# Optimization experiments

Hardware: AMD Instinct MI355X
Metric: run time of the kernel (lower is better)

Reference implementation:

```python
import jax, jax.numpy as jnp
import numpy as np

B, N, F_IN, H, E = 8, 10000, 128, 128, 160000


def setup_inputs() -> dict:
    key = jax.random.key(0)
    ks = jax.random.split(key, 6)
    x = jax.random.normal(ks[0], (B, N, F_IN), dtype=jnp.float32)
    edge_index = jax.random.randint(ks[1], (2, E), 0, N, dtype=jnp.int64)
    # GCNConv params (glorot-ish scale), LayerNorm affine params
    W1 = jax.random.normal(ks[2], (F_IN, H), dtype=jnp.float32) / np.sqrt(F_IN)
    b1 = jnp.zeros((H,), dtype=jnp.float32)
    W2 = jax.random.normal(ks[3], (H, H), dtype=jnp.float32) / np.sqrt(H)
    b2 = jnp.zeros((H,), dtype=jnp.float32)
    ln_w = jnp.ones((H,), dtype=jnp.float32)
    ln_b = jnp.zeros((H,), dtype=jnp.float32)
    return {"x": x, "edge_index": edge_index, "W1": W1, "b1": b1,
            "W2": W2, "b2": b2, "ln_w": ln_w, "ln_b": ln_b}


def reference(x, edge_index, W1, b1, W2, b2, ln_w, ln_b):
    # x: [B, N, F]; edge_index: [2, E] shared across batch (tiled per graph
    # in the original via node offsets -> equivalent to vmapping over batch).
    n = x.shape[1]
    loops = jnp.arange(n, dtype=edge_index.dtype)
    src = jnp.concatenate([edge_index[0], loops])  # add self-loops (GCNConv default)
    dst = jnp.concatenate([edge_index[1], loops])
    # symmetric degree normalization: deg over targets with self-loops
    deg = jax.ops.segment_sum(jnp.ones(dst.shape[0], dtype=x.dtype), dst, num_segments=n)
    dinv = jnp.where(deg > 0, jax.lax.rsqrt(deg), 0.0)
    w_e = dinv[src] * dinv[dst]  # [E+N] per-edge norm

    def gcn_agg(h):  # h: [B, N, H] -> gather, scale, scatter-add
        msg = h[:, src, :] * w_e[None, :, None]  # [B, E+N, H]
        return jax.vmap(lambda m: jax.ops.segment_sum(m, dst, num_segments=n))(msg)

    h1 = jax.nn.relu(gcn_agg(x @ W1) + b1)
    h2 = gcn_agg(h1 @ W2) + b2
    # LayerNorm over last dim (eps=1e-5, torch default)
    mu = jnp.mean(h2, axis=-1, keepdims=True)
    var = jnp.mean(jnp.square(h2 - mu), axis=-1, keepdims=True)
    out = (h2 - mu) * jax.lax.rsqrt(var + 1e-5) * ln_w + ln_b
    return out  # [B, N, H]
```

## Files before the change

kernel.cpp:

```cpp
#include <hip/hip_runtime.h>
#include <hip/hip_bf16.h>

#define NNODES 10000
#define NB 8
#define NF 128
#define NE 160000

typedef __attribute__((ext_vector_type(8))) short  short8;
typedef __attribute__((ext_vector_type(8))) unsigned short ushort8;
typedef __attribute__((ext_vector_type(4))) float  f32x4;

__device__ __forceinline__ unsigned short f2b(float f) {
    union { float f; unsigned u; } v; v.f = f;
    unsigned r = v.u + 0x7FFF + ((v.u >> 16) & 1);
    return (unsigned short)(r >> 16);
}
__device__ __forceinline__ unsigned int f2b2(float a, float b) {
    union { __hip_bfloat162 h; unsigned int u; } v;
    v.h = __float22bfloat162_rn(make_float2(a, b));
    return v.u;
}
__device__ __forceinline__ float b2f_lo(unsigned u) {
    union { unsigned u; float f; } v; v.u = u << 16; return v.f;
}
__device__ __forceinline__ float b2f_hi(unsigned u) {
    union { unsigned u; float f; } v; v.u = u & 0xffff0000u; return v.f;
}


__global__ void k_count(const int* __restrict__ ei, int* __restrict__ cnt) {
    int e = blockIdx.x * blockDim.x + threadIdx.x;
    if (e < NE) atomicAdd(&cnt[ei[NE + e]], 1);
}

__global__ __launch_bounds__(1024) void k_scan(const int* __restrict__ cnt,
                                               int* __restrict__ row_ptr,
                                               float* __restrict__ dinv) {
    __shared__ int wsum[16];
    const int t = threadIdx.x;
    const int lane = t & 63, wv = t >> 6;
    const int CH = 10;
    int lo = t * CH;
    int hi = min(lo + CH, NNODES);
    int c10[CH];
    int s = 0;
    for (int i = lo; i < hi; i++) {
        int c = cnt[i];
        c10[i - lo] = c;
        dinv[i] = rsqrtf((float)(c + 1));
        s += c;
    }
    int v = s;
    #pragma unroll
    for (int m = 1; m < 64; m <<= 1) {
        int o = __shfl_up(v, m);
        if (lane >= m) v += o;
    }
    if (lane == 63) wsum[wv] = v;
    __syncthreads();
    if (t < 16) {
        int w = wsum[t];
        #pragma unroll
        for (int m = 1; m < 16; m <<= 1) {
            int o = __shfl_up(w, m);
            if (t >= m) w += o;
        }
        wsum[t] = w;
    }
    __syncthreads();
    int base = v - s + (wv ? wsum[wv - 1] : 0);
    for (int i = lo; i < hi; i++) { row_ptr[i] = base; base += c10[i - lo]; }
    if (t == 1023) row_ptr[NNODES] = wsum[15];
}

__global__ void k_scatter(const int* __restrict__ ei, const int* __restrict__ row_ptr,
                          int* __restrict__ fill, const float* __restrict__ dinv,
                          unsigned int* __restrict__ edge) {
    int e = blockIdx.x * blockDim.x + threadIdx.x;
    if (e >= NE) return;
    int s = ei[e];
    int d = ei[NE + e];
    int pos = row_ptr[d] + atomicAdd(&fill[d], 1);
    edge[pos] = (unsigned)s | ((unsigned)f2b(dinv[s] * dinv[d]) << 16);
}

__global__ void k_wt2(const float* __restrict__ W1, unsigned short* __restrict__ Wt1,
                      const float* __restrict__ W2, unsigned short* __restrict__ Wt2) {
    int bid = blockIdx.x;
    const float* W = (bid < 64) ? W1 : W2;
    unsigned short* Wt = (bid < 64) ? Wt1 : Wt2;
    int id = (bid & 63) * 256 + threadIdx.x;
    int n = id >> 7, k = id & 127;
    Wt[(size_t)n * 128 + k] = f2b(W[(size_t)k * 128 + n]);
}

template <bool ABF16>
__global__ __launch_bounds__(256) void k_mm_mfma(const void* __restrict__ Ap,
                                                 const unsigned short* __restrict__ Wt,
                                                 unsigned short* __restrict__ Cn) {
    __shared__ unsigned short clds[128 * 136];
    const int t = threadIdx.x;
    const int wid = t >> 6, lane = t & 63;
    const int quad = lane >> 4, l16 = lane & 15;
    const int m0 = blockIdx.x * 128 + (wid & 1) * 64;
    const int nb = (wid >> 1) * 64;
    const int kq = quad * 8;

    f32x4 acc[4][4] = {};

    #pragma unroll
    for (int ks = 0; ks < 128; ks += 32) {
        short8 af[4];
        #pragma unroll
        for (int ni = 0; ni < 4; ni++)
            af[ni] = *(const short8*)(Wt + (size_t)(nb + ni * 16 + l16) * 128 + ks + kq);
        short8 bf[4];
        #pragma unroll
        for (int mi = 0; mi < 4; mi++) {
            const size_t row = (size_t)(m0 + mi * 16 + l16);
            if constexpr (ABF16) {
                bf[mi] = *(const short8*)((const unsigned short*)Ap + row * 128 + ks + kq);
            } else {
                const float* p = (const float*)Ap + row * 128 + ks + kq;
                float4 u0 = *(const float4*)p;
                float4 u1 = *(const float4*)(p + 4);
                union { uint4 u4; short8 s8; } cv;
                cv.u4.x = f2b2(u0.x, u0.y); cv.u4.y = f2b2(u0.z, u0.w);
                cv.u4.z = f2b2(u1.x, u1.y); cv.u4.w = f2b2(u1.z, u1.w);
                bf[mi] = cv.s8;
            }
        }
        #pragma unroll
        for (int mi = 0; mi < 4; mi++)
            #pragma unroll
            for (int ni = 0; ni < 4; ni++)
                acc[mi][ni] = __builtin_amdgcn_mfma_f32_16x16x32_bf16(
                    af[ni], bf[mi], acc[mi][ni], 0, 0, 0);
    }

    {
        const int rbase = (wid & 1) * 64;
        #pragma unroll
        for (int mi = 0; mi < 4; mi++) {
            int rr = rbase + mi * 16 + l16;
            #pragma unroll
            for (int ni = 0; ni < 4; ni++) {
                uint2 p;
                p.x = f2b2(acc[mi][ni][0], acc[mi][ni][1]);
                p.y = f2b2(acc[mi][ni][2], acc[mi][ni][3]);
                *(uint2*)(clds + rr * 136 + nb + ni * 16 + quad * 4) = p;
            }
        }
    }
    __syncthreads();
    {
        const int r = t >> 1, h = t & 1;
        size_t gm = (size_t)blockIdx.x * 128 + r;
        unsigned short* dst = Cn + gm * 128 + h * 64;
        const unsigned short* srow = clds + r * 136 + h * 64;
        #pragma unroll
        for (int i = 0; i < 8; i++)
            *(ushort8*)(dst + i * 8) = *(const ushort8*)(srow + i * 8);
    }
}


__global__ __launch_bounds__(256) void k_agg_relu(const unsigned int* __restrict__ hNu,
                                                  const float* __restrict__ bias,
                                                  const int* __restrict__ row_ptr,
                                                  const unsigned int* __restrict__ edge,
                                                  const float* __restrict__ dinv,
                                                  unsigned int* __restrict__ h1u) {
    const int t = threadIdx.x;
    const int b = blockIdx.x & 7;
    const int g = blockIdx.x >> 3;
    const int wid = __builtin_amdgcn_readfirstlane(t >> 6);
    const int lane = t & 63;
    const int n = g * 4 + wid;

    const unsigned int* base = hNu + (size_t)b * NNODES * 64 + lane;
    float di = dinv[n];
    float wself = di * di;
    unsigned int u = base[(size_t)n * 64];
    float a0 = b2f_lo(u) * wself;
    float a1 = b2f_hi(u) * wself;

    int e = row_ptr[n], e1 = row_ptr[n + 1];
    for (; e + 8 <= e1; e += 8) {
        unsigned int E[8];
        #pragma unroll
        for (int j = 0; j < 8; j++) E[j] = edge[e + j];
        unsigned int U[8];
        #pragma unroll
        for (int j = 0; j < 8; j++) U[j] = base[(size_t)(E[j] & 0xffffu) * 64];
        #pragma unroll
        for (int j = 0; j < 8; j++) {
            float w = b2f_hi(E[j]);
            a0 = fmaf(b2f_lo(U[j]), w, a0);
            a1 = fmaf(b2f_hi(U[j]), w, a1);
        }
    }
    for (; e + 4 <= e1; e += 4) {
        unsigned int E[4];
        #pragma unroll
        for (int j = 0; j < 4; j++) E[j] = edge[e + j];
        unsigned int U[4];
        #pragma unroll
        for (int j = 0; j < 4; j++) U[j] = base[(size_t)(E[j] & 0xffffu) * 64];
        #pragma unroll
        for (int j = 0; j < 4; j++) {
            float w = b2f_hi(E[j]);
            a0 = fmaf(b2f_lo(U[j]), w, a0);
            a1 = fmaf(b2f_hi(U[j]), w, a1);
        }
    }
    for (; e < e1; ++e) {
        unsigned int E = edge[e];
        float w = b2f_hi(E);
        unsigned int uu = base[(size_t)(E & 0xffffu) * 64];
        a0 = fmaf(b2f_lo(uu), w, a0);
        a1 = fmaf(b2f_hi(uu), w, a1);
    }
    a0 = fmaxf(a0 + bias[lane * 2], 0.f);
    a1 = fmaxf(a1 + bias[lane * 2 + 1], 0.f);
    __builtin_nontemporal_store(f2b2(a0, a1), &h1u[((size_t)b * NNODES + n) * 64 + lane]);
}

__global__ __launch_bounds__(256) void k_agg_ln(const unsigned int* __restrict__ hNu,
                                                const float* __restrict__ bias,
                                                const int* __restrict__ row_ptr,
                                                const unsigned int* __restrict__ edge,
                                                const float* __restrict__ dinv,
                                                const float* __restrict__ ln_w,
                                                const float* __restrict__ ln_b,
                                                float* __restrict__ out) {
    const int t = threadIdx.x;
    const int b = blockIdx.x & 7;
    const int g = blockIdx.x >> 3;
    const int wid = __builtin_amdgcn_readfirstlane(t >> 6);
    const int lane = t & 63;
    const int n = g * 4 + wid;

    const unsigned int* base = hNu + (size_t)b * NNODES * 64 + lane;
    float di = dinv[n];
    float wself = di * di;
    unsigned int u = base[(size_t)n * 64];
    float a0 = b2f_lo(u) * wself;
    float a1 = b2f_hi(u) * wself;

    int e = row_ptr[n], e1 = row_ptr[n + 1];
    for (; e + 8 <= e1; e += 8) {
        unsigned int E[8];
        #pragma unroll
        for (int j = 0; j < 8; j++) E[j] = edge[e + j];
        unsigned int U[8];
        #pragma unroll
        for (int j = 0; j < 8; j++) U[j] = base[(size_t)(E[j] & 0xffffu) * 64];
        #pragma unroll
        for (int j = 0; j < 8; j++) {
            float w = b2f_hi(E[j]);
            a0 = fmaf(b2f_lo(U[j]), w, a0);
            a1 = fmaf(b2f_hi(U[j]), w, a1);
        }
    }
    for (; e + 4 <= e1; e += 4) {
        unsigned int E[4];
        #pragma unroll
        for (int j = 0; j < 4; j++) E[j] = edge[e + j];
        unsigned int U[4];
        #pragma unroll
        for (int j = 0; j < 4; j++) U[j] = base[(size_t)(E[j] & 0xffffu) * 64];
        #pragma unroll
        for (int j = 0; j < 4; j++) {
            float w = b2f_hi(E[j]);
            a0 = fmaf(b2f_lo(U[j]), w, a0);
            a1 = fmaf(b2f_hi(U[j]), w, a1);
        }
    }
    for (; e < e1; ++e) {
        unsigned int E = edge[e];
        float w = b2f_hi(E);
        unsigned int uu = base[(size_t)(E & 0xffffu) * 64];
        a0 = fmaf(b2f_lo(uu), w, a0);
        a1 = fmaf(b2f_hi(uu), w, a1);
    }
    a0 += bias[lane * 2];
    a1 += bias[lane * 2 + 1];

    float s1 = a0 + a1;
    float s2 = a0 * a0 + a1 * a1;
    #pragma unroll
    for (int m = 1; m < 64; m <<= 1) {
        s1 += __shfl_xor(s1, m);
        s2 += __shfl_xor(s2, m);
    }
    float mu = s1 * (1.f / NF);
    float var = s2 * (1.f / NF) - mu * mu;
    float rs = rsqrtf(var + 1e-5f);

    float o0 = (a0 - mu) * rs * ln_w[lane * 2] + ln_b[lane * 2];
    float o1 = (a1 - mu) * rs * ln_w[lane * 2 + 1] + ln_b[lane * 2 + 1];
    float* dst = out + ((size_t)b * NNODES + n) * 128 + lane * 2;
    __builtin_nontemporal_store(o0, dst);
    __builtin_nontemporal_store(o1, dst + 1);
}


extern "C" void kernel_launch(void* const* d_in, const int* in_sizes, int n_in,
                              void* d_out, int out_size, void* d_ws, size_t ws_size,
                              hipStream_t stream) {
    const float* x    = (const float*)d_in[0];
    const int*   ei   = (const int*)d_in[1];
    const float* W1   = (const float*)d_in[2];
    const float* b1   = (const float*)d_in[3];
    const float* W2   = (const float*)d_in[4];
    const float* b2   = (const float*)d_in[5];
    const float* ln_w = (const float*)d_in[6];
    const float* ln_b = (const float*)d_in[7];
    float* out = (float*)d_out;

    char* ws = (char*)d_ws;
    int*            cnt     = (int*)(ws + 0);
    int*            fill    = (int*)(ws + 40192);
    int*            row_ptr = (int*)(ws + 80384);
    float*          dinv    = (float*)(ws + 120832);
    unsigned int*   edge    = (unsigned int*)(ws + 161024);
    unsigned short* hA16    = (unsigned short*)(ws + 1441024);
    unsigned short* h1b     = (unsigned short*)(ws + 21921024);
    unsigned short* Wt1     = (unsigned short*)cnt;
    unsigned short* Wt2     = (unsigned short*)fill;

    hipMemsetAsync(ws, 0, 80384, stream);
    k_count  <<<(NE + 255) / 256, 256, 0, stream>>>(ei, cnt);
    k_scan   <<<1, 1024, 0, stream>>>(cnt, row_ptr, dinv);
    k_scatter<<<(NE + 255) / 256, 256, 0, stream>>>(ei, row_ptr, fill, dinv, edge);
    k_wt2    <<<128, 256, 0, stream>>>(W1, Wt1, W2, Wt2);

    k_mm_mfma<false><<<(NB * NNODES) / 128, 256, 0, stream>>>(x, Wt1, hA16);
    k_agg_relu<<<(NNODES / 4) * NB, 256, 0, stream>>>((const unsigned int*)hA16, b1,
                                                      row_ptr, edge, dinv,
                                                      (unsigned int*)h1b);

    k_mm_mfma<true><<<(NB * NNODES) / 128, 256, 0, stream>>>(h1b, Wt2, hA16);
    k_agg_ln<<<(NNODES / 4) * NB, 256, 0, stream>>>((const unsigned int*)hA16, b2,
                                                    row_ptr, edge, dinv,
                                                    ln_w, ln_b, out);
}
```

Baseline: 233.4 us.

## Assign aggregation batches to XCDs via atomic work claiming for L2 locality

```diff
diff --git a/kernel.cpp b/kernel.cpp
--- a/kernel.cpp
+++ b/kernel.cpp
@@ -5,10 +5,13 @@
 #define NB 8
 #define NF 128
 #define NE 160000
+#define NGRP 625
 
 typedef __attribute__((ext_vector_type(8))) short  short8;
 typedef __attribute__((ext_vector_type(8))) unsigned short ushort8;
 typedef __attribute__((ext_vector_type(4))) float  f32x4;
+
+#define HWREG_XCC_ID (20 | (0 << 6) | ((4 - 1) << 11))
 
 __device__ __forceinline__ unsigned short f2b(float f) {
     union { float f; unsigned u; } v; v.f = f;
@@ -28,9 +31,21 @@
 }
 
 
-__global__ void k_count(const int* __restrict__ ei, int* __restrict__ cnt) {
-    int e = blockIdx.x * blockDim.x + threadIdx.x;
-    if (e < NE) atomicAdd(&cnt[ei[NE + e]], 1);
+__global__ void k_count_wt(const int* __restrict__ ei, int* __restrict__ cnt,
+                           const float* __restrict__ W1, unsigned short* __restrict__ Wt1,
+                           const float* __restrict__ W2, unsigned short* __restrict__ Wt2) {
+    int bid = blockIdx.x;
+    if (bid < 625) {
+        int e = bid * 256 + threadIdx.x;
+        atomicAdd(&cnt[ei[NE + e]], 1);
+    } else {
+        int id2 = (bid - 625) * 256 + threadIdx.x;
+        const float* W = (id2 < 16384) ? W1 : W2;
+        unsigned short* Wt = (id2 < 16384) ? Wt1 : Wt2;
+        int id = id2 & 16383;
+        int n = id >> 7, k = id & 127;
+        Wt[n * 128 + k] = f2b(W[k * 128 + n]);
+    }
 }
 
 __global__ __launch_bounds__(1024) void k_scan(const int* __restrict__ cnt,
@@ -84,16 +99,6 @@
     edge[pos] = (unsigned)s | ((unsigned)f2b(dinv[s] * dinv[d]) << 16);
 }
 
-__global__ void k_wt2(const float* __restrict__ W1, unsigned short* __restrict__ Wt1,
-                      const float* __restrict__ W2, unsigned short* __restrict__ Wt2) {
-    int bid = blockIdx.x;
-    const float* W = (bid < 64) ? W1 : W2;
-    unsigned short* Wt = (bid < 64) ? Wt1 : Wt2;
-    int id = (bid & 63) * 256 + threadIdx.x;
-    int n = id >> 7, k = id & 127;
-    Wt[(size_t)n * 128 + k] = f2b(W[(size_t)k * 128 + n]);
-}
-
 template <bool ABF16>
 __global__ __launch_bounds__(256) void k_mm_mfma(const void* __restrict__ Ap,
                                                  const unsigned short* __restrict__ Wt,
@@ -165,65 +170,86 @@
 }
 
 
+__device__ __forceinline__ int claim_item(int* ctr) {
+    int xcc = __builtin_amdgcn_s_getreg(HWREG_XCC_ID) & 7;
+    int got = -1;
+    for (int k = 0; k < 8; k++) {
+        int b = (xcc + k) & 7;
+        int idx = atomicAdd(&ctr[b], 1);
+        if (idx < NGRP) { got = b * NGRP + idx; break; }
+    }
+    return got;
+}
+
 __global__ __launch_bounds__(256) void k_agg_relu(const unsigned int* __restrict__ hNu,
                                                   const float* __restrict__ bias,
                                                   const int* __restrict__ row_ptr,
                                                   const unsigned int* __restrict__ edge,
                                                   const float* __restrict__ dinv,
-                                                  unsigned int* __restrict__ h1u) {
-    const int t = threadIdx.x;
-    const int b = blockIdx.x & 7;
-    const int g = blockIdx.x >> 3;
-    const int wid = __builtin_amdgcn_readfirstlane(t >> 6);
-    const int lane = t & 63;
-    const int n = g * 4 + wid;
+                                                  unsigned int* __restrict__ h1u,
+                                                  int* __restrict__ ctr) {
+    __shared__ int s_item;
+    if (threadIdx.x == 0) s_item = claim_item(ctr);
+    __syncthreads();
+    const int item = s_item;
+    if (item < 0) return;
+    const int b = item / NGRP;
+    const int g = item - b * NGRP;
+    const int wid = __builtin_amdgcn_readfirstlane(threadIdx.x >> 6);
+    const int lane = threadIdx.x & 63;
 
     const unsigned int* base = hNu + (size_t)b * NNODES * 64 + lane;
-    float di = dinv[n];
-    float wself = di * di;
-    unsigned int u = base[(size_t)n * 64];
-    float a0 = b2f_lo(u) * wself;
-    float a1 = b2f_hi(u) * wself;
-
-    int e = row_ptr[n], e1 = row_ptr[n + 1];
-    for (; e + 8 <= e1; e += 8) {
-        unsigned int E[8];
-        #pragma unroll
-        for (int j = 0; j < 8; j++) E[j] = edge[e + j];
-        unsigned int U[8];
-        #pragma unroll
-        for (int j = 0; j < 8; j++) U[j] = base[(size_t)(E[j] & 0xffffu) * 64];
-        #pragma unroll
-        for (int j = 0; j < 8; j++) {
-            float w = b2f_hi(E[j]);
-            a0 = fmaf(b2f_lo(U[j]), w, a0);
-            a1 = fmaf(b2f_hi(U[j]), w, a1);
-        }
-    }
-    for (; e + 4 <= e1; e += 4) {
-        unsigned int E[4];
-        #pragma unroll
-        for (int j = 0; j < 4; j++) E[j] = edge[e + j];
-        unsigned int U[4];
-        #pragma unroll
-        for (int j = 0; j < 4; j++) U[j] = base[(size_t)(E[j] & 0xffffu) * 64];
-        #pragma unroll
-        for (int j = 0; j < 4; j++) {
-            float w = b2f_hi(E[j]);
-            a0 = fmaf(b2f_lo(U[j]), w, a0);
-            a1 = fmaf(b2f_hi(U[j]), w, a1);
-        }
-    }
-    for (; e < e1; ++e) {
-        unsigned int E = edge[e];
-        float w = b2f_hi(E);
-        unsigned int uu = base[(size_t)(E & 0xffffu) * 64];
-        a0 = fmaf(b2f_lo(uu), w, a0);
-        a1 = fmaf(b2f_hi(uu), w, a1);
-    }
-    a0 = fmaxf(a0 + bias[lane * 2], 0.f);
-    a1 = fmaxf(a1 + bias[lane * 2 + 1], 0.f);
-    __builtin_nontemporal_store(f2b2(a0, a1), &h1u[((size_t)b * NNODES + n) * 64 + lane]);
+    const float bias0 = bias[lane * 2], bias1 = bias[lane * 2 + 1];
+
+    for (int q = 0; q < 4; q++) {
+        const int n = g * 16 + wid * 4 + q;
+        float di = dinv[n];
+        float wself = di * di;
+        unsigned int u = base[(size_t)n * 64];
+        float a0 = b2f_lo(u) * wself;
+        float a1 = b2f_hi(u) * wself;
+
+        int e = row_ptr[n], e1 = row_ptr[n + 1];
+        for (; e + 8 <= e1; e += 8) {
+            unsigned int E[8];
+            #pragma unroll
+            for (int j = 0; j < 8; j++) E[j] = edge[e + j];
+            unsigned int U[8];
+            #pragma unroll
+            for (int j = 0; j < 8; j++) U[j] = base[(size_t)(E[j] & 0xffffu) * 64];
+            #pragma unroll
+            for (int j = 0; j < 8; j++) {
+                float w = b2f_hi(E[j]);
+                a0 = fmaf(b2f_lo(U[j]), w, a0);
+                a1 = fmaf(b2f_hi(U[j]), w, a1);
+            }
+        }
+        for (; e + 4 <= e1; e += 4) {
+            unsigned int E[4];
+            #pragma unroll
+            for (int j = 0; j < 4; j++) E[j] = edge[e + j];
+            unsigned int U[4];
+            #pragma unroll
+            for (int j = 0; j < 4; j++) U[j] = base[(size_t)(E[j] & 0xffffu) * 64];
+            #pragma unroll
+            for (int j = 0; j < 4; j++) {
+                float w = b2f_hi(E[j]);
+                a0 = fmaf(b2f_lo(U[j]), w, a0);
+                a1 = fmaf(b2f_hi(U[j]), w, a1);
+            }
+        }
+        for (; e < e1; ++e) {
+            unsigned int E = edge[e];
+            float w = b2f_hi(E);
+            unsigned int uu = base[(size_t)(E & 0xffffu) * 64];
+            a0 = fmaf(b2f_lo(uu), w, a0);
+            a1 = fmaf(b2f_hi(uu), w, a1);
+        }
+        a0 = fmaxf(a0 + bias0, 0.f);
+        a1 = fmaxf(a1 + bias1, 0.f);
+        __builtin_nontemporal_store(f2b2(a0, a1),
+                                    &h1u[((size_t)b * NNODES + n) * 64 + lane]);
+    }
 }
 
 __global__ __launch_bounds__(256) void k_agg_ln(const unsigned int* __restrict__ hNu,
@@ -233,76 +259,87 @@
                                                 const float* __restrict__ dinv,
                                                 const float* __restrict__ ln_w,
                                                 const float* __restrict__ ln_b,
-                                                float* __restrict__ out) {
-    const int t = threadIdx.x;
-    const int b = blockIdx.x & 7;
-    const int g = blockIdx.x >> 3;
-    const int wid = __builtin_amdgcn_readfirstlane(t >> 6);
-    const int lane = t & 63;
-    const int n = g * 4 + wid;
+                                                float* __restrict__ out,
+                                                int* __restrict__ ctr) {
+    __shared__ int s_item;
+    if (threadIdx.x == 0) s_item = claim_item(ctr);
+    __syncthreads();
+    const int item = s_item;
+    if (item < 0) return;
+    const int b = item / NGRP;
+    const int g = item - b * NGRP;
+    const int wid = __builtin_amdgcn_readfirstlane(threadIdx.x >> 6);
+    const int lane = threadIdx.x & 63;
 
     const unsigned int* base = hNu + (size_t)b * NNODES * 64 + lane;
-    float di = dinv[n];
-    float wself = di * di;
-    unsigned int u = base[(size_t)n * 64];
-    float a0 = b2f_lo(u) * wself;
-    float a1 = b2f_hi(u) * wself;
-
-    int e = row_ptr[n], e1 = row_ptr[n + 1];
-    for (; e + 8 <= e1; e += 8) {
-        unsigned int E[8];
-        #pragma unroll
-        for (int j = 0; j < 8; j++) E[j] = edge[e + j];
-        unsigned int U[8];
-        #pragma unroll
-        for (int j = 0; j < 8; j++) U[j] = base[(size_t)(E[j] & 0xffffu) * 64];
-        #pragma unroll
-        for (int j = 0; j < 8; j++) {
-            float w = b2f_hi(E[j]);
-            a0 = fmaf(b2f_lo(U[j]), w, a0);
-            a1 = fmaf(b2f_hi(U[j]), w, a1);
-        }
-    }
-    for (; e + 4 <= e1; e += 4) {
-        unsigned int E[4];
-        #pragma unroll
-        for (int j = 0; j < 4; j++) E[j] = edge[e + j];
-        unsigned int U[4];
-        #pragma unroll
-        for (int j = 0; j < 4; j++) U[j] = base[(size_t)(E[j] & 0xffffu) * 64];
-        #pragma unroll
-        for (int j = 0; j < 4; j++) {
-            float w = b2f_hi(E[j]);
-            a0 = fmaf(b2f_lo(U[j]), w, a0);
-            a1 = fmaf(b2f_hi(U[j]), w, a1);
-        }
-    }
-    for (; e < e1; ++e) {
-        unsigned int E = edge[e];
-        float w = b2f_hi(E);
-        unsigned int uu = base[(size_t)(E & 0xffffu) * 64];
-        a0 = fmaf(b2f_lo(uu), w, a0);
-        a1 = fmaf(b2f_hi(uu), w, a1);
-    }
-    a0 += bias[lane * 2];
-    a1 += bias[lane * 2 + 1];
-
-    float s1 = a0 + a1;
-    float s2 = a0 * a0 + a1 * a1;
-    #pragma unroll
-    for (int m = 1; m < 64; m <<= 1) {
-        s1 += __shfl_xor(s1, m);
-        s2 += __shfl_xor(s2, m);
-    }
-    float mu = s1 * (1.f / NF);
-    float var = s2 * (1.f / NF) - mu * mu;
-    float rs = rsqrtf(var + 1e-5f);
-
-    float o0 = (a0 - mu) * rs * ln_w[lane * 2] + ln_b[lane * 2];
-    float o1 = (a1 - mu) * rs * ln_w[lane * 2 + 1] + ln_b[lane * 2 + 1];
-    float* dst = out + ((size_t)b * NNODES + n) * 128 + lane * 2;
-    __builtin_nontemporal_store(o0, dst);
-    __builtin_nontemporal_store(o1, dst + 1);
+    const float bias0 = bias[lane * 2], bias1 = bias[lane * 2 + 1];
+    const float lnw0 = ln_w[lane * 2], lnw1 = ln_w[lane * 2 + 1];
+    const float lnb0 = ln_b[lane * 2], lnb1 = ln_b[lane * 2 + 1];
+
+    for (int q = 0; q < 4; q++) {
+        const int n = g * 16 + wid * 4 + q;
+        float di = dinv[n];
+        float wself = di * di;
+        unsigned int u = base[(size_t)n * 64];
+        float a0 = b2f_lo(u) * wself;
+        float a1 = b2f_hi(u) * wself;
+
+        int e = row_ptr[n], e1 = row_ptr[n + 1];
+        for (; e + 8 <= e1; e += 8) {
+            unsigned int E[8];
+            #pragma unroll
+            for (int j = 0; j < 8; j++) E[j] = edge[e + j];
+            unsigned int U[8];
+            #pragma unroll
+            for (int j = 0; j < 8; j++) U[j] = base[(size_t)(E[j] & 0xffffu) * 64];
+            #pragma unroll
+            for (int j = 0; j < 8; j++) {
+                float w = b2f_hi(E[j]);
+                a0 = fmaf(b2f_lo(U[j]), w, a0);
+                a1 = fmaf(b2f_hi(U[j]), w, a1);
+            }
+        }
+        for (; e + 4 <= e1; e += 4) {
+            unsigned int E[4];
+            #pragma unroll
+            for (int j = 0; j < 4; j++) E[j] = edge[e + j];
+            unsigned int U[4];
+            #pragma unroll
+            for (int j = 0; j < 4; j++) U[j] = base[(size_t)(E[j] & 0xffffu) * 64];
+            #pragma unroll
+            for (int j = 0; j < 4; j++) {
+                float w = b2f_hi(E[j]);
+                a0 = fmaf(b2f_lo(U[j]), w, a0);
+                a1 = fmaf(b2f_hi(U[j]), w, a1);
+            }
+        }
+        for (; e < e1; ++e) {
+            unsigned int E = edge[e];
+            float w = b2f_hi(E);
+            unsigned int uu = base[(size_t)(E & 0xffffu) * 64];
+            a0 = fmaf(b2f_lo(uu), w, a0);
+            a1 = fmaf(b2f_hi(uu), w, a1);
+        }
+        a0 += bias0;
+        a1 += bias1;
+
+        float s1 = a0 + a1;
+        float s2 = a0 * a0 + a1 * a1;
+        #pragma unroll
+        for (int m = 1; m < 64; m <<= 1) {
+            s1 += __shfl_xor(s1, m);
+            s2 += __shfl_xor(s2, m);
+        }
+        float mu = s1 * (1.f / NF);
+        float var = s2 * (1.f / NF) - mu * mu;
+        float rs = rsqrtf(var + 1e-5f);
+
+        float o0 = (a0 - mu) * rs * lnw0 + lnb0;
+        float o1 = (a1 - mu) * rs * lnw1 + lnb1;
+        float* dst = out + ((size_t)b * NNODES + n) * 128 + lane * 2;
+        __builtin_nontemporal_store(o0, dst);
+        __builtin_nontemporal_store(o1, dst + 1);
+    }
 }
 
 
@@ -322,27 +359,28 @@
     char* ws = (char*)d_ws;
     int*            cnt     = (int*)(ws + 0);
     int*            fill    = (int*)(ws + 40192);
-    int*            row_ptr = (int*)(ws + 80384);
-    float*          dinv    = (float*)(ws + 120832);
-    unsigned int*   edge    = (unsigned int*)(ws + 161024);
+    int*            ctrA    = (int*)(ws + 80384);
+    int*            ctrB    = (int*)(ws + 80416);
+    int*            row_ptr = (int*)(ws + 80448);
+    float*          dinv    = (float*)(ws + 120512);
+    unsigned int*   edge    = (unsigned int*)(ws + 160512);
+    unsigned short* Wt1     = (unsigned short*)(ws + 800512);
+    unsigned short* Wt2     = (unsigned short*)(ws + 833280);
     unsigned short* hA16    = (unsigned short*)(ws + 1441024);
     unsigned short* h1b     = (unsigned short*)(ws + 21921024);
-    unsigned short* Wt1     = (unsigned short*)cnt;
-    unsigned short* Wt2     = (unsigned short*)fill;
-
-    hipMemsetAsync(ws, 0, 80384, stream);
-    k_count  <<<(NE + 255) / 256, 256, 0, stream>>>(ei, cnt);
-    k_scan   <<<1, 1024, 0, stream>>>(cnt, row_ptr, dinv);
-    k_scatter<<<(NE + 255) / 256, 256, 0, stream>>>(ei, row_ptr, fill, dinv, edge);
-    k_wt2    <<<128, 256, 0, stream>>>(W1, Wt1, W2, Wt2);
+
+    hipMemsetAsync(ws, 0, 80448, stream);
+    k_count_wt<<<753, 256, 0, stream>>>(ei, cnt, W1, Wt1, W2, Wt2);
+    k_scan    <<<1, 1024, 0, stream>>>(cnt, row_ptr, dinv);
+    k_scatter <<<(NE + 255) / 256, 256, 0, stream>>>(ei, row_ptr, fill, dinv, edge);
 
     k_mm_mfma<false><<<(NB * NNODES) / 128, 256, 0, stream>>>(x, Wt1, hA16);
-    k_agg_relu<<<(NNODES / 4) * NB, 256, 0, stream>>>((const unsigned int*)hA16, b1,
-                                                      row_ptr, edge, dinv,
-                                                      (unsigned int*)h1b);
+    k_agg_relu<<<NB * NGRP, 256, 0, stream>>>((const unsigned int*)hA16, b1,
+                                              row_ptr, edge, dinv,
+                                              (unsigned int*)h1b, ctrA);
 
     k_mm_mfma<true><<<(NB * NNODES) / 128, 256, 0, stream>>>(h1b, Wt2, hA16);
-    k_agg_ln<<<(NNODES / 4) * NB, 256, 0, stream>>>((const unsigned int*)hA16, b2,
-                                                    row_ptr, edge, dinv,
-                                                    ln_w, ln_b, out);
-}
+    k_agg_ln<<<NB * NGRP, 256, 0, stream>>>((const unsigned int*)hA16, b2,
+                                            row_ptr, edge, dinv,
+                                            ln_w, ln_b, out, ctrB);
+}
```

Measured after the change: 314.3 us. 1.35x slower.
